# Performance work log

Measured on AMD Instinct MI355X. Metric: run time of the kernel, lower is better.

## Reference

```python
import jax, jax.numpy as jnp
import numpy as np

D_MODEL = 1024
NUM_HEADS = 16
HEAD_DIM = D_MODEL // NUM_HEADS
CAUSAL = True


def rope_cos_sin(seq_len, dim):
    inv_freq = 1.0 / (10000.0 ** (jnp.arange(0, dim, 2, dtype=jnp.float32) / dim))
    t = jnp.arange(seq_len, dtype=jnp.float32)
    freqs = jnp.einsum('i,j->ij', t, inv_freq)          # [S, dim/2]
    emb = jnp.concatenate([freqs, freqs], axis=-1)      # [S, dim]
    return jnp.cos(emb), jnp.sin(emb)


def rotate_half(x):
    x1, x2 = jnp.split(x, 2, axis=-1)
    return jnp.concatenate([-x2, x1], axis=-1)


def setup_inputs() -> dict:
    key = jax.random.key(0)
    k1, k2, k3, k4, k5 = jax.random.split(key, 5)
    B, S = 2, 2048
    x = jax.random.normal(k1, (B, S, D_MODEL), dtype=jnp.float32)
    s = 1.0 / np.sqrt(D_MODEL)
    W_qkv = jax.random.normal(k2, (D_MODEL, 3 * D_MODEL), dtype=jnp.float32) * s
    b_qkv = jax.random.normal(k3, (3 * D_MODEL,), dtype=jnp.float32) * 0.01
    W_out = jax.random.normal(k4, (D_MODEL, D_MODEL), dtype=jnp.float32) * s
    b_out = jax.random.normal(k5, (D_MODEL,), dtype=jnp.float32) * 0.01
    return {"x": x, "W_qkv": W_qkv, "b_qkv": b_qkv, "W_out": W_out, "b_out": b_out}


def reference(x, W_qkv, b_qkv, W_out, b_out):
    B, S, _ = x.shape
    qkv = x @ W_qkv + b_qkv                              # [B, S, 3D]
    q, k, v = jnp.split(qkv, 3, axis=-1)
    # [B, H, S, hd]
    q = q.reshape(B, S, NUM_HEADS, HEAD_DIM).transpose(0, 2, 1, 3)
    k = k.reshape(B, S, NUM_HEADS, HEAD_DIM).transpose(0, 2, 1, 3)
    v = v.reshape(B, S, NUM_HEADS, HEAD_DIM).transpose(0, 2, 1, 3)
    cos, sin = rope_cos_sin(S, HEAD_DIM)                 # [S, hd]
    cos = cos[None, None]
    sin = sin[None, None]
    q = q * cos + rotate_half(q) * sin
    k = k * cos + rotate_half(k) * sin
    scores = jnp.einsum('bhqd,bhkd->bhqk', q, k) / np.sqrt(HEAD_DIM)
    if CAUSAL:
        causal_mask = jnp.triu(jnp.ones((S, S), dtype=bool), k=1)
        scores = jnp.where(causal_mask, -jnp.inf, scores)
    attn = jax.nn.softmax(scores, axis=-1)
    out = jnp.einsum('bhqk,bhkd->bhqd', attn, v)         # [B, H, S, hd]
    out = out.transpose(0, 2, 1, 3).reshape(B, S, D_MODEL)
    return out @ W_out + b_out
```

## Files before the change

### kernel.cpp

```cpp
#include <hip/hip_runtime.h>
#include <hip/hip_bf16.h>
#include <math.h>

typedef __bf16 bf16;
typedef __bf16 bf16x8 __attribute__((ext_vector_type(8)));
typedef unsigned short ushort8 __attribute__((ext_vector_type(8)));
typedef float floatx4 __attribute__((ext_vector_type(4)));

#define MFMA_BF16(a, b, c) __builtin_amdgcn_mfma_f32_16x16x32_bf16(a, b, c, 0, 0, 0)

#define Q_SCALE 0.18033688011112042f
#define NEG_INVFREQ_LOG2 0.41524101186092029f
#define INV_2PI 0.15915494309189535f

#if __has_builtin(__builtin_amdgcn_exp2f)
#define EXP2F(x) __builtin_amdgcn_exp2f(x)
#else
#define EXP2F(x) exp2f(x)
#endif

__device__ __forceinline__ void hw_sincos_rev(float rev, float* sn, float* cs) {
#if __has_builtin(__builtin_amdgcn_sinf) && __has_builtin(__builtin_amdgcn_cosf) && \
    __has_builtin(__builtin_amdgcn_fractf)
  const float f = __builtin_amdgcn_fractf(rev);
  *sn = __builtin_amdgcn_sinf(f);
  *cs = __builtin_amdgcn_cosf(f);
#else
  sincosf(rev * 6.2831853071795864f, sn, cs);
#endif
}

__device__ __forceinline__ bf16x8 cvt8(const float4 a, const float4 b) {
  bf16x8 t;
  t[0] = (bf16)a.x; t[1] = (bf16)a.y; t[2] = (bf16)a.z; t[3] = (bf16)a.w;
  t[4] = (bf16)b.x; t[5] = (bf16)b.y; t[6] = (bf16)b.z; t[7] = (bf16)b.w;
  return t;
}

__device__ __forceinline__ unsigned int pack2(float a, float b) {
#if __has_builtin(__builtin_amdgcn_cvt_pk_bf16_f32)
  return __builtin_bit_cast(unsigned int, __builtin_amdgcn_cvt_pk_bf16_f32(a, b));
#else
  unsigned short lo = __builtin_bit_cast(unsigned short, (bf16)a);
  unsigned short hi = __builtin_bit_cast(unsigned short, (bf16)b);
  return (unsigned int)lo | ((unsigned int)hi << 16);
#endif
}

__device__ __forceinline__ void gld16(const bf16* g, bf16* l) {
  __builtin_amdgcn_global_load_lds(
      (const __attribute__((address_space(1))) unsigned int*)g,
      (__attribute__((address_space(3))) unsigned int*)l, 16, 0, 0);
}

__device__ __forceinline__ void transpose_tile(const float* __restrict__ in,
                                               bf16* __restrict__ out, int N,
                                               int bx, int by, int t,
                                               bf16 (*T)[40]) {
  const int k0 = by * 32, n0 = bx * 64;
  {
    const int k = t >> 3, n8 = (t & 7) * 8;
    const float* p = &in[(size_t)(k0 + k) * N + n0 + n8];
    const float4 a = *(const float4*)p;
    const float4 b = *(const float4*)(p + 4);
    const float v[8] = {a.x, a.y, a.z, a.w, b.x, b.y, b.z, b.w};
#pragma unroll
    for (int j = 0; j < 8; j++) {
      const int n = n8 + j;
      T[n][k ^ (8 * ((n >> 3) & 3))] = (bf16)v[j];
    }
  }
  __syncthreads();
  {
    const int n = t >> 2, k8 = (t & 3) * 8;
    const int kp = k8 ^ (8 * ((n >> 3) & 3));
    *(bf16x8*)&out[(size_t)(n0 + n) * 1024 + k0 + k8] = *(const bf16x8*)&T[n][kp];
  }
}

__global__ __launch_bounds__(256) void prep_kernel(
    const float* __restrict__ x, bf16* __restrict__ xb,
    const float* __restrict__ Wq, bf16* __restrict__ Wqt,
    const float* __restrict__ Wo, bf16* __restrict__ Wot) {
  __shared__ __align__(16) bf16 T[64][40];
  const int bid = blockIdx.x, t = threadIdx.x;
  if (bid < 2048) {
    const int i = bid * 256 + t;
    const float4 a = *(const float4*)&x[(size_t)i * 8];
    const float4 b = *(const float4*)&x[(size_t)i * 8 + 4];
    *(bf16x8*)&xb[(size_t)i * 8] = cvt8(a, b);
  } else if (bid < 3584) {
    const int bb = bid - 2048;
    transpose_tile(Wq, Wqt, 3072, bb % 48, bb / 48, t, T);
  } else {
    const int bb = bid - 3584;
    transpose_tile(Wo, Wot, 1024, bb % 16, bb / 16, t, T);
  }
}

template <int TN, int MODE>
__global__ __launch_bounds__(256) void gemm_kernel(
    const bf16* __restrict__ A, const bf16* __restrict__ Bt,
    const float* __restrict__ bias, void* __restrict__ out0,
    bf16* __restrict__ outK, bf16* __restrict__ outV, int M, int N, int K) {
  constexpr int NI = TN / 32;
  constexpr int BI = TN / 32;
  __shared__ __align__(16) bf16 As2[2][128][32];
  __shared__ __align__(16) bf16 Bs2[2][TN][32];

  const int tid = threadIdx.x, lane = tid & 63, w = tid >> 6;
  const int c = lane & 15, quad = lane >> 4;
  const int wm = w >> 1, wn = w & 1;
  const int m0 = blockIdx.y * 128, n0 = blockIdx.x * TN;
  const int srow = lane >> 2, scol = (lane & 3) * 8;

  floatx4 acc[4][NI] = {};

  for (int k0 = 0; k0 < K; k0 += 64) {
    __syncthreads();
#pragma unroll
    for (int i = 0; i < 4; i++) {
      const int seg = w * 4 + i;
      const int kh = seg >> 3, r0 = (seg & 7) * 16;
      gld16(&A[(size_t)(m0 + r0 + srow) * K + k0 + kh * 32 + scol],
            &As2[kh][r0][0]);
    }
#pragma unroll
    for (int i = 0; i < BI; i++) {
      const int seg = w * BI + i;
      const int kh = seg / (TN / 16), r0 = (seg % (TN / 16)) * 16;
      gld16(&Bt[(size_t)(n0 + r0 + srow) * K + k0 + kh * 32 + scol],
            &Bs2[kh][r0][0]);
    }
    __syncthreads();

#pragma unroll
    for (int kh = 0; kh < 2; kh++) {
      bf16x8 af[4], bfr[NI];
#pragma unroll
      for (int mi = 0; mi < 4; mi++)
        af[mi] = *(const bf16x8*)&As2[kh][wm * 64 + mi * 16 + c][quad * 8];
#pragma unroll
      for (int ni = 0; ni < NI; ni++)
        bfr[ni] = *(const bf16x8*)&Bs2[kh][wn * (TN / 2) + ni * 16 + c][quad * 8];
#pragma unroll
      for (int mi = 0; mi < 4; mi++)
#pragma unroll
        for (int ni = 0; ni < NI; ni++)
          acc[mi][ni] = MFMA_BF16(af[mi], bfr[ni], acc[mi][ni]);
    }
  }

  if (MODE == 0) {
#pragma unroll
    for (int mi = 0; mi < 4; mi++)
#pragma unroll
      for (int ni = 0; ni < NI; ni++)
#pragma unroll
        for (int r = 0; r < 4; r++) {
          const int row = m0 + wm * 64 + mi * 16 + quad * 4 + r;
          const int col = n0 + wn * (TN / 2) + ni * 16 + c;
          ((float*)out0)[(size_t)row * N + col] = acc[mi][ni][r] + bias[col];
        }
  } else {
    const int colb = n0 + wn * (TN / 2);
    const int t = colb >> 10;
    const int h = (colb & 1023) >> 6;
    bf16* dst = (t == 0) ? (bf16*)out0 : (t == 1 ? outK : outV);
    if (t == 2) {
#pragma unroll
      for (int mi = 0; mi < 4; mi++)
#pragma unroll
        for (int ni = 0; ni < NI; ni++)
#pragma unroll
          for (int r = 0; r < 4; r++) {
            const int row = m0 + wm * 64 + mi * 16 + quad * 4 + r;
            const int col = colb + ni * 16 + c;
            const int b = row >> 11, s = row & 2047;
            dst[(((size_t)b * 16 + h) * 2048 + s) * 64 + (col & 63)] =
                (bf16)(acc[mi][ni][r] + bias[col]);
          }
    } else {
      const float qs = (t == 0) ? Q_SCALE : 1.0f;
      const float invr[2] = {exp2f(-NEG_INVFREQ_LOG2 * (float)c) * INV_2PI,
                             exp2f(-NEG_INVFREQ_LOG2 * (float)(16 + c)) * INV_2PI};
#pragma unroll
      for (int mi = 0; mi < 4; mi++) {
#pragma unroll
        for (int r = 0; r < 4; r++) {
          const int row = m0 + wm * 64 + mi * 16 + quad * 4 + r;
          const int b = row >> 11, s = row & 2047;
          const size_t base = (((size_t)b * 16 + h) * 2048 + s) * 64;
#pragma unroll
          for (int ni = 0; ni < 2; ni++) {
            float sn, cs;
            hw_sincos_rev((float)s * invr[ni], &sn, &cs);
            const float v1 = acc[mi][ni][r] + bias[colb + ni * 16 + c];
            const float v2 = acc[mi][ni + 2][r] + bias[colb + (ni + 2) * 16 + c];
            const int d = ni * 16 + c;
            dst[base + d] = (bf16)((v1 * cs - v2 * sn) * qs);
            dst[base + d + 32] = (bf16)((v2 * cs + v1 * sn) * qs);
          }
        }
      }
    }
  }
}

struct AttnState {
  floatx4 o[4];
  float l;
};

__device__ __forceinline__ void attn_step(
    const bf16x8 qf[2], const bf16x8 kf[4][2], const bf16x8 vf[4][2],
    bf16 (*PsW)[72], AttnState& st, int qglob, int kbase, bool diag, int c,
    int quad) {
  floatx4 sacc[4] = {};
#pragma unroll
  for (int kg = 0; kg < 4; kg++)
#pragma unroll
    for (int dh = 0; dh < 2; dh++)
      sacc[kg] = MFMA_BF16(kf[kg][dh], qf[dh], sacc[kg]);

#pragma unroll
  for (int kg = 0; kg < 4; kg++) {
    float p[4];
#pragma unroll
    for (int r = 0; r < 4; r++) {
      float e = EXP2F(sacc[kg][r]);
      if (diag && (kbase + kg * 16 + quad * 4 + r > qglob)) e = 0.0f;
      p[r] = e;
    }
    st.l += (p[0] + p[1]) + (p[2] + p[3]);
    const uint2 u = {pack2(p[0], p[1]), pack2(p[2], p[3])};
    *(uint2*)&PsW[c][kg * 16 + quad * 4] = u;
  }

  bf16x8 pf[2];
#pragma unroll
  for (int ks = 0; ks < 2; ks++)
    pf[ks] = *(const bf16x8*)&PsW[c][ks * 32 + quad * 8];

#pragma unroll
  for (int dg = 0; dg < 4; dg++)
#pragma unroll
    for (int ks = 0; ks < 2; ks++)
      st.o[dg] = MFMA_BF16(vf[dg][ks], pf[ks], st.o[dg]);
}

__global__ __launch_bounds__(256) void attn_part_kernel(
    const bf16* __restrict__ Q, const bf16* __restrict__ K,
    const bf16* __restrict__ V, float* __restrict__ Opart,
    float* __restrict__ Lpart) {
  const int S = 2048;
  const int p = blockIdx.x;
  const int j = blockIdx.y;
  const int bh = blockIdx.z;
  const int tid = threadIdx.x, lane = tid & 63, wave = tid >> 6;
  const int c = lane & 15, quad = lane >> 4;

  __shared__ __align__(16) bf16 Ks2[2][64][32];
  __shared__ __align__(16) bf16 Vt[64][72];
  __shared__ __align__(16) bf16 Ps[4][16][72];

  const bf16* Qb = Q + (size_t)bh * S * 64;
  const bf16* Kb = K + (size_t)bh * S * 64;
  const bf16* Vb = V + (size_t)bh * S * 64;

  const int qA = p, qB = 31 - p;
  const int qgA = qA * 64 + wave * 16 + c;
  const int qgB = qB * 64 + wave * 16 + c;

  bf16x8 qfA[2], qfB[2];
#pragma unroll
  for (int dh = 0; dh < 2; dh++) {
    qfA[dh] = *(const bf16x8*)&Qb[(size_t)qgA * 64 + dh * 32 + quad * 8];
    qfB[dh] = *(const bf16x8*)&Qb[(size_t)qgB * 64 + dh * 32 + quad * 8];
  }

  AttnState stA = {}, stB = {};

  const int vcc = (tid & 7) * 8;
  const int vr2 = ((tid >> 3) + 4 * (tid & 7)) & 31;
  const int ksr = lane >> 2, ksc = (lane & 3) * 8;

  for (int kt = j; kt <= qB; kt += 2) {
    __syncthreads();
#pragma unroll
    for (int i = 0; i < 2; i++) {
      const int seg = wave * 2 + i;
      const int dh = seg >> 2, r0 = (seg & 3) * 16;
      gld16(&Kb[(size_t)(kt * 64 + r0 + ksr) * 64 + dh * 32 + ksc],
            &Ks2[dh][r0][0]);
    }
    {
      const bf16* vs = &Vb[(size_t)(kt * 64 + 2 * vr2) * 64 + vcc];
      const ushort8 w0 = __builtin_bit_cast(ushort8, *(const bf16x8*)vs);
      const ushort8 w1 = __builtin_bit_cast(ushort8, *(const bf16x8*)(vs + 64));
#pragma unroll
      for (int jj = 0; jj < 8; jj++)
        *(unsigned int*)&Vt[vcc + jj][2 * vr2] =
            (unsigned int)w0[jj] | ((unsigned int)w1[jj] << 16);
    }
    __syncthreads();

    bf16x8 kf[4][2];
#pragma unroll
    for (int kg = 0; kg < 4; kg++)
#pragma unroll
      for (int dh = 0; dh < 2; dh++)
        kf[kg][dh] = *(const bf16x8*)&Ks2[dh][kg * 16 + c][quad * 8];

    bf16x8 vf[4][2];
#pragma unroll
    for (int dg = 0; dg < 4; dg++)
#pragma unroll
      for (int ks = 0; ks < 2; ks++)
        vf[dg][ks] = *(const bf16x8*)&Vt[dg * 16 + c][ks * 32 + quad * 8];

    attn_step(qfB, kf, vf, Ps[wave], stB, qgB, kt * 64, kt == qB, c, quad);
    if (kt <= qA)
      attn_step(qfA, kf, vf, Ps[wave], stA, qgA, kt * 64, kt == qA, c, quad);
  }

  stA.l += __shfl_xor(stA.l, 16);
  stA.l += __shfl_xor(stA.l, 32);
  stB.l += __shfl_xor(stB.l, 16);
  stB.l += __shfl_xor(stB.l, 32);

  float* Ob = Opart + ((size_t)j * 32 + bh) * S * 64;
  float* Lb = Lpart + ((size_t)j * 32 + bh) * S;
#pragma unroll
  for (int dg = 0; dg < 4; dg++) {
    *(floatx4*)&Ob[(size_t)qgA * 64 + dg * 16 + quad * 4] = stA.o[dg];
    *(floatx4*)&Ob[(size_t)qgB * 64 + dg * 16 + quad * 4] = stB.o[dg];
  }
  if (quad == 0) {
    Lb[qgA] = stA.l;
    Lb[qgB] = stB.l;
  }
}

__global__ __launch_bounds__(256) void merge_kernel(
    const float* __restrict__ Opart, const float* __restrict__ Lpart,
    bf16* __restrict__ AO) {
  const int t = blockIdx.x * 256 + threadIdx.x;
  const int d4 = t & 15;
  const int q = (t >> 4) & 2047;
  const int bh = t >> 15;
  const size_t half = (size_t)32 * 2048 * 64;
  const size_t off = ((size_t)bh * 2048 + q) * 64 + d4 * 4;
  const float4 o0 = *(const float4*)&Opart[off];
  const float4 o1 = *(const float4*)&Opart[half + off];
  const float iv = 1.0f / (Lpart[bh * 2048 + q] + Lpart[32 * 2048 + bh * 2048 + q]);
  const int b = bh >> 4, h = bh & 15;
  const uint2 u = {pack2((o0.x + o1.x) * iv, (o0.y + o1.y) * iv),
                   pack2((o0.z + o1.z) * iv, (o0.w + o1.w) * iv)};
  *(uint2*)&AO[((size_t)(b * 2048 + q)) * 1024 + h * 64 + d4 * 4] = u;
}

extern "C" void kernel_launch(void* const* d_in, const int* in_sizes, int n_in,
                              void* d_out, int out_size, void* d_ws,
                              size_t ws_size, hipStream_t stream) {
  const float* x = (const float*)d_in[0];
  const float* W_qkv = (const float*)d_in[1];
  const float* b_qkv = (const float*)d_in[2];
  const float* W_out = (const float*)d_in[3];
  const float* b_out = (const float*)d_in[4];
  float* out = (float*)d_out;

  const size_t qn = (size_t)2 * 16 * 2048 * 64;

  bf16* xb = (bf16*)d_ws;
  bf16* Wqkvt = xb + qn;
  bf16* Wot = Wqkvt + 3072 * 1024;
  bf16* Qw = Wot + 1024 * 1024;
  bf16* Kw = Qw + qn;
  bf16* Vw = Kw + qn;
  float* Opart = (float*)(Vw + qn);
  float* Lpart = Opart + 2 * (size_t)32 * 2048 * 64;
  bf16* AO = xb;

  prep_kernel<<<dim3(4096), 256, 0, stream>>>(x, xb, W_qkv, Wqkvt, W_out, Wot);
  gemm_kernel<128, 1><<<dim3(3072 / 128, 4096 / 128), 256, 0, stream>>>(
      xb, Wqkvt, b_qkv, Qw, Kw, Vw, 4096, 3072, 1024);
  attn_part_kernel<<<dim3(16, 2, 32), 256, 0, stream>>>(Qw, Kw, Vw, Opart, Lpart);
  merge_kernel<<<dim3(4096), 256, 0, stream>>>(Opart, Lpart, AO);
  gemm_kernel<64, 0><<<dim3(1024 / 64, 4096 / 128), 256, 0, stream>>>(
      AO, Wot, b_out, out, nullptr, nullptr, 4096, 1024, 1024);
}
```

Measured before the change: 204.6 us.

## Merge split-K attention partials inside one 512-thread block via shared memory

The two key-split attention partials were previously computed by separate blocks, written to global memory in fp32, and combined by a separate merge kernel. Now one 512-thread block holds both halves as two 4-wave groups, and the groups combine their outputs and row sums through shared memory before writing bf16 directly. This removes the fp32 partial round trip through global memory and one kernel launch. In exchange the grid has half as many blocks, each with more shared memory and threads, so fewer blocks may fit per CU and the __syncthreads now span both groups.

```diff
diff --git a/kernel.cpp b/kernel.cpp
--- a/kernel.cpp
+++ b/kernel.cpp
@@ -249,28 +249,30 @@
       st.o[dg] = MFMA_BF16(vf[dg][ks], pf[ks], st.o[dg]);
 }
 
-__global__ __launch_bounds__(256) void attn_part_kernel(
-    const bf16* __restrict__ Q, const bf16* __restrict__ K,
-    const bf16* __restrict__ V, float* __restrict__ Opart,
-    float* __restrict__ Lpart) {
+__global__ __launch_bounds__(512) void attn_kernel(const bf16* __restrict__ Q,
+                                                   const bf16* __restrict__ K,
+                                                   const bf16* __restrict__ V,
+                                                   bf16* __restrict__ Aout) {
   const int S = 2048;
   const int p = blockIdx.x;
-  const int j = blockIdx.y;
-  const int bh = blockIdx.z;
+  const int bh = blockIdx.y;
   const int tid = threadIdx.x, lane = tid & 63, wave = tid >> 6;
+  const int g = wave >> 2, w4 = wave & 3;
   const int c = lane & 15, quad = lane >> 4;
-
-  __shared__ __align__(16) bf16 Ks2[2][64][32];
-  __shared__ __align__(16) bf16 Vt[64][72];
-  __shared__ __align__(16) bf16 Ps[4][16][72];
+  const int tg = tid & 255;
+
+  __shared__ __align__(16) char smem[53248];
+  bf16* Ksg = (bf16*)(smem + g * 17408);
+  bf16* Vtg = (bf16*)(smem + g * 17408 + 8192);
+  bf16(*PsW)[72] = (bf16(*)[72])(smem + 34816 + wave * 2304);
 
   const bf16* Qb = Q + (size_t)bh * S * 64;
   const bf16* Kb = K + (size_t)bh * S * 64;
   const bf16* Vb = V + (size_t)bh * S * 64;
 
   const int qA = p, qB = 31 - p;
-  const int qgA = qA * 64 + wave * 16 + c;
-  const int qgB = qB * 64 + wave * 16 + c;
+  const int qgA = qA * 64 + w4 * 16 + c;
+  const int qgB = qB * 64 + w4 * 16 + c;
 
   bf16x8 qfA[2], qfB[2];
 #pragma unroll
@@ -281,47 +283,55 @@
 
   AttnState stA = {}, stB = {};
 
-  const int vcc = (tid & 7) * 8;
-  const int vr2 = ((tid >> 3) + 4 * (tid & 7)) & 31;
+  const int vcc = (tg & 7) * 8;
+  const int vr2 = ((tg >> 3) + 4 * (tg & 7)) & 31;
   const int ksr = lane >> 2, ksc = (lane & 3) * 8;
 
-  for (int kt = j; kt <= qB; kt += 2) {
+  const int nit = (qB + 2) >> 1;
+  for (int it = 0; it < nit; it++) {
+    const int kt = 2 * it + g;
+    const bool active = (kt <= qB);
     __syncthreads();
-#pragma unroll
-    for (int i = 0; i < 2; i++) {
-      const int seg = wave * 2 + i;
-      const int dh = seg >> 2, r0 = (seg & 3) * 16;
-      gld16(&Kb[(size_t)(kt * 64 + r0 + ksr) * 64 + dh * 32 + ksc],
-            &Ks2[dh][r0][0]);
-    }
-    {
-      const bf16* vs = &Vb[(size_t)(kt * 64 + 2 * vr2) * 64 + vcc];
-      const ushort8 w0 = __builtin_bit_cast(ushort8, *(const bf16x8*)vs);
-      const ushort8 w1 = __builtin_bit_cast(ushort8, *(const bf16x8*)(vs + 64));
-#pragma unroll
-      for (int jj = 0; jj < 8; jj++)
-        *(unsigned int*)&Vt[vcc + jj][2 * vr2] =
-            (unsigned int)w0[jj] | ((unsigned int)w1[jj] << 16);
+    if (active) {
+#pragma unroll
+      for (int i = 0; i < 2; i++) {
+        const int seg = w4 * 2 + i;
+        const int dh = seg >> 2, r0 = (seg & 3) * 16;
+        gld16(&Kb[(size_t)(kt * 64 + r0 + ksr) * 64 + dh * 32 + ksc],
+              &Ksg[dh * 2048 + r0 * 32]);
+      }
+      {
+        const bf16* vs = &Vb[(size_t)(kt * 64 + 2 * vr2) * 64 + vcc];
+        const ushort8 w0 = __builtin_bit_cast(ushort8, *(const bf16x8*)vs);
+        const ushort8 w1 = __builtin_bit_cast(ushort8, *(const bf16x8*)(vs + 64));
+#pragma unroll
+        for (int jj = 0; jj < 8; jj++)
+          *(unsigned int*)&Vtg[(vcc + jj) * 72 + 2 * vr2] =
+              (unsigned int)w0[jj] | ((unsigned int)w1[jj] << 16);
+      }
     }
     __syncthreads();
-
-    bf16x8 kf[4][2];
-#pragma unroll
-    for (int kg = 0; kg < 4; kg++)
-#pragma unroll
-      for (int dh = 0; dh < 2; dh++)
-        kf[kg][dh] = *(const bf16x8*)&Ks2[dh][kg * 16 + c][quad * 8];
-
-    bf16x8 vf[4][2];
-#pragma unroll
-    for (int dg = 0; dg < 4; dg++)
-#pragma unroll
-      for (int ks = 0; ks < 2; ks++)
-        vf[dg][ks] = *(const bf16x8*)&Vt[dg * 16 + c][ks * 32 + quad * 8];
-
-    attn_step(qfB, kf, vf, Ps[wave], stB, qgB, kt * 64, kt == qB, c, quad);
-    if (kt <= qA)
-      attn_step(qfA, kf, vf, Ps[wave], stA, qgA, kt * 64, kt == qA, c, quad);
+    if (active) {
+      bf16x8 kf[4][2];
+#pragma unroll
+      for (int kg = 0; kg < 4; kg++)
+#pragma unroll
+        for (int dh = 0; dh < 2; dh++)
+          kf[kg][dh] =
+              *(const bf16x8*)&Ksg[dh * 2048 + (kg * 16 + c) * 32 + quad * 8];
+
+      bf16x8 vf[4][2];
+#pragma unroll
+      for (int dg = 0; dg < 4; dg++)
+#pragma unroll
+        for (int ks = 0; ks < 2; ks++)
+          vf[dg][ks] =
+              *(const bf16x8*)&Vtg[(dg * 16 + c) * 72 + ks * 32 + quad * 8];
+
+      attn_step(qfB, kf, vf, PsW, stB, qgB, kt * 64, kt == qB, c, quad);
+      if (kt <= qA)
+        attn_step(qfA, kf, vf, PsW, stA, qgA, kt * 64, kt == qA, c, quad);
+    }
   }
 
   stA.l += __shfl_xor(stA.l, 16);
@@ -329,35 +339,47 @@
   stB.l += __shfl_xor(stB.l, 16);
   stB.l += __shfl_xor(stB.l, 32);
 
-  float* Ob = Opart + ((size_t)j * 32 + bh) * S * 64;
-  float* Lb = Lpart + ((size_t)j * 32 + bh) * S;
-#pragma unroll
-  for (int dg = 0; dg < 4; dg++) {
-    *(floatx4*)&Ob[(size_t)qgA * 64 + dg * 16 + quad * 4] = stA.o[dg];
-    *(floatx4*)&Ob[(size_t)qgB * 64 + dg * 16 + quad * 4] = stB.o[dg];
-  }
-  if (quad == 0) {
-    Lb[qgA] = stA.l;
-    Lb[qgB] = stB.l;
-  }
-}
-
-__global__ __launch_bounds__(256) void merge_kernel(
-    const float* __restrict__ Opart, const float* __restrict__ Lpart,
-    bf16* __restrict__ AO) {
-  const int t = blockIdx.x * 256 + threadIdx.x;
-  const int d4 = t & 15;
-  const int q = (t >> 4) & 2047;
-  const int bh = t >> 15;
-  const size_t half = (size_t)32 * 2048 * 64;
-  const size_t off = ((size_t)bh * 2048 + q) * 64 + d4 * 4;
-  const float4 o0 = *(const float4*)&Opart[off];
-  const float4 o1 = *(const float4*)&Opart[half + off];
-  const float iv = 1.0f / (Lpart[bh * 2048 + q] + Lpart[32 * 2048 + bh * 2048 + q]);
-  const int b = bh >> 4, h = bh & 15;
-  const uint2 u = {pack2((o0.x + o1.x) * iv, (o0.y + o1.y) * iv),
-                   pack2((o0.z + o1.z) * iv, (o0.w + o1.w) * iv)};
-  *(uint2*)&AO[((size_t)(b * 2048 + q)) * 1024 + h * 64 + d4 * 4] = u;
+  float* OsA = (float*)smem;
+  float* OsB = (float*)(smem + 17408);
+  float* LsA = (float*)(smem + 34816);
+  float* LsB = (float*)(smem + 35072);
+  const int qrow = w4 * 16 + c;
+
+  __syncthreads();
+  if (g == 1) {
+#pragma unroll
+    for (int dg = 0; dg < 4; dg++) {
+      *(floatx4*)&OsA[qrow * 68 + dg * 16 + quad * 4] = stA.o[dg];
+      *(floatx4*)&OsB[qrow * 68 + dg * 16 + quad * 4] = stB.o[dg];
+    }
+    if (quad == 0) {
+      LsA[qrow] = stA.l;
+      LsB[qrow] = stB.l;
+    }
+  }
+  __syncthreads();
+  if (g == 0) {
+#pragma unroll
+    for (int dg = 0; dg < 4; dg++) {
+      stA.o[dg] += *(const floatx4*)&OsA[qrow * 68 + dg * 16 + quad * 4];
+      stB.o[dg] += *(const floatx4*)&OsB[qrow * 68 + dg * 16 + quad * 4];
+    }
+    const float ivA = 1.0f / (stA.l + LsA[qrow]);
+    const float ivB = 1.0f / (stB.l + LsB[qrow]);
+
+    const int b = bh >> 4, h = bh & 15;
+#pragma unroll
+    for (int dg = 0; dg < 4; dg++) {
+      const uint2 uA = {pack2(stA.o[dg][0] * ivA, stA.o[dg][1] * ivA),
+                        pack2(stA.o[dg][2] * ivA, stA.o[dg][3] * ivA)};
+      const uint2 uB = {pack2(stB.o[dg][0] * ivB, stB.o[dg][1] * ivB),
+                        pack2(stB.o[dg][2] * ivB, stB.o[dg][3] * ivB)};
+      *(uint2*)&Aout[((size_t)b * 2048 + qgA) * 1024 + h * 64 + dg * 16 +
+                     quad * 4] = uA;
+      *(uint2*)&Aout[((size_t)b * 2048 + qgB) * 1024 + h * 64 + dg * 16 +
+                     quad * 4] = uB;
+    }
+  }
 }
 
 extern "C" void kernel_launch(void* const* d_in, const int* in_sizes, int n_in,
@@ -378,15 +400,12 @@
   bf16* Qw = Wot + 1024 * 1024;
   bf16* Kw = Qw + qn;
   bf16* Vw = Kw + qn;
-  float* Opart = (float*)(Vw + qn);
-  float* Lpart = Opart + 2 * (size_t)32 * 2048 * 64;
   bf16* AO = xb;
 
   prep_kernel<<<dim3(4096), 256, 0, stream>>>(x, xb, W_qkv, Wqkvt, W_out, Wot);
   gemm_kernel<128, 1><<<dim3(3072 / 128, 4096 / 128), 256, 0, stream>>>(
       xb, Wqkvt, b_qkv, Qw, Kw, Vw, 4096, 3072, 1024);
-  attn_part_kernel<<<dim3(16, 2, 32), 256, 0, stream>>>(Qw, Kw, Vw, Opart, Lpart);
-  merge_kernel<<<dim3(4096), 256, 0, stream>>>(Opart, Lpart, AO);
+  attn_kernel<<<dim3(16, 32), 512, 0, stream>>>(Qw, Kw, Vw, AO);
   gemm_kernel<64, 0><<<dim3(1024 / 64, 4096 / 128), 256, 0, stream>>>(
       AO, Wot, b_out, out, nullptr, nullptr, 4096, 1024, 1024);
 }
```

Measured after the change: 208.6 us. Within noise of the previous version (+2.0%).
